# Kernel tuning notes

Measured on AMD Instinct MI355X. Metric: run time of the kernel, lower is better.

Reference implementation:

```python
import jax, jax.numpy as jnp
import numpy as np

TOKENS, IN_F, OUT_F = 8192, 4096, 4096
ZERO_POINT = 0      # input zero point (int8)
OUT_ZP = 0          # output zero point (int8)
OUT_SCALE = 0.05    # output quant scale


def setup_inputs() -> dict:
    key = jax.random.key(0)
    k1, k2, k3, k4 = jax.random.split(key, 4)
    x = jax.random.randint(k1, (TOKENS, IN_F), -128, 128, dtype=jnp.int32).astype(jnp.int8)
    # weight stored as [in_features, out_features] (module.weight.t() quantized in from_float)
    weight = jax.random.randint(k2, (IN_F, OUT_F), -127, 128, dtype=jnp.int32).astype(jnp.int8)
    bias = jax.random.randint(k3, (1, OUT_F), -1000, 1000, dtype=jnp.int32)
    gemm_scales = jax.random.uniform(k4, (1, OUT_F), minval=1e-4, maxval=2e-4, dtype=jnp.float32)
    return {"x": x, "weight": weight, "bias": bias, "gemm_scales": gemm_scales}


def reference(x, weight, bias, gemm_scales):
    # int8 -> int32 -> fp32, subtract input zero point
    a = (x.astype(jnp.int32) - ZERO_POINT).astype(jnp.float32)   # [T, IN]
    w = weight.astype(jnp.float32)                               # [IN, OUT]
    gemm_o = (a @ w + bias.astype(jnp.float32)) * gemm_scales / OUT_SCALE  # [T, OUT]
    out = jnp.clip(gemm_o + OUT_ZP, -128, 127).astype(jnp.int8)
    return out
```

## Files before the change

### kernel.cpp

```cpp
#include <hip/hip_runtime.h>
#include <stdint.h>

#define TOKENS 8192
#define IN_F   4096
#define OUT_F  4096

#define BM 256
#define BN 256
#define BK 64
#define NK (IN_F / BK)
#define THREADS 512

typedef int v4i __attribute__((ext_vector_type(4)));

#define GLOBAL_AS __attribute__((address_space(1)))
#define LDS_AS    __attribute__((address_space(3)))

__global__ __launch_bounds__(256) void pack_x_kernel(const int* __restrict__ x32,
                                                     uint8_t* __restrict__ x8) {
  int t = blockIdx.x * 256 + threadIdx.x;
  const int4 v = ((const int4*)x32)[t];
  uint32_t p = (uint32_t)(v.x & 0xFF)
             | ((uint32_t)(v.y & 0xFF) << 8)
             | ((uint32_t)(v.z & 0xFF) << 16)
             | ((uint32_t)(v.w & 0xFF) << 24);
  ((uint32_t*)x8)[t] = p;
}

__global__ __launch_bounds__(256) void packT_w_kernel(const int* __restrict__ w32,
                                                      uint8_t* __restrict__ wt8) {
  int tn = (blockIdx.x & 63) * 64;
  int tk = (blockIdx.x >> 6) * 64;
  int t = threadIdx.x;
  int n  = tn + (t >> 2);
  int k0 = tk + (t & 3) * 16;
  uint32_t words[4];
#pragma unroll
  for (int w = 0; w < 4; ++w) {
    uint32_t acc = 0;
#pragma unroll
    for (int j = 0; j < 4; ++j) {
      int val = w32[(size_t)(k0 + w * 4 + j) * OUT_F + n];
      acc |= (uint32_t)(val & 0xFF) << (8 * j);
    }
    words[w] = acc;
  }
  uint4 o = make_uint4(words[0], words[1], words[2], words[3]);
  *(uint4*)(wt8 + (size_t)n * IN_F + k0) = o;
}

__global__ __launch_bounds__(THREADS, 2) void gemm_i8_kernel(const uint8_t* __restrict__ A,
                                                             const uint8_t* __restrict__ BT,
                                                             const int* __restrict__ bias,
                                                             const float* __restrict__ scales,
                                                             int* __restrict__ out) {
  __shared__ __align__(16) uint8_t lds[4 * 32768];

  const int t    = threadIdx.x;
  const int lane = t & 63;
  const int w    = t >> 6;
  const int wr   = w >> 2;
  const int wc   = w & 3;
  const int fr   = lane & 15;
  const int fq   = lane >> 4;

  int bid = blockIdx.x;
  int swz = (bid & 7) * 64 + (bid >> 3);
  int bm = swz >> 4;
  int bn = swz & 15;

  const int lsz  = t ^ ((t >> 3) & 7);
  const int srow = lsz >> 2;
  const int scol = (lsz & 3) * 16;
  const size_t gA0 = (size_t)(bm * BM + srow) * IN_F + scol;
  const size_t gA1 = gA0 + (size_t)128 * IN_F;
  const size_t gB0 = (size_t)(bn * BN + srow) * IN_F + scol;
  const size_t gB1 = gB0 + (size_t)128 * IN_F;
  const int ldst = t * 16;

  auto stage = [&](int j) {
    uint8_t* sb = lds + (j & 3) * 32768;
    const int k0 = j * BK;
    __builtin_amdgcn_global_load_lds((const GLOBAL_AS void*)(A  + gA0 + k0),
                                     (LDS_AS void*)(sb + ldst),           16, 0, 0);
    __builtin_amdgcn_global_load_lds((const GLOBAL_AS void*)(A  + gA1 + k0),
                                     (LDS_AS void*)(sb + 8192  + ldst),   16, 0, 0);
    __builtin_amdgcn_global_load_lds((const GLOBAL_AS void*)(BT + gB0 + k0),
                                     (LDS_AS void*)(sb + 16384 + ldst),   16, 0, 0);
    __builtin_amdgcn_global_load_lds((const GLOBAL_AS void*)(BT + gB1 + k0),
                                     (LDS_AS void*)(sb + 24576 + ldst),   16, 0, 0);
  };

  int aoff[8], boff[4];
#pragma unroll
  for (int m = 0; m < 8; ++m) {
    int row = wr * 128 + m * 16 + fr;
    int half = row >> 7, rl = row & 127;
    int b = rl * 64 + fq * 16;
    b ^= ((rl >> 1) & 7) << 4;
    aoff[m] = half * 8192 + b;
  }
#pragma unroll
  for (int n = 0; n < 4; ++n) {
    int row = wc * 64 + n * 16 + fr;
    int half = row >> 7, rl = row & 127;
    int b = rl * 64 + fq * 16;
    b ^= ((rl >> 1) & 7) << 4;
    boff[n] = 16384 + half * 8192 + b;
  }

  v4i acc[8][4];
  const v4i vzero = {0, 0, 0, 0};
#pragma unroll
  for (int m = 0; m < 8; ++m)
#pragma unroll
    for (int n = 0; n < 4; ++n) acc[m][n] = vzero;

  auto compute = [&](int i) {
    const uint8_t* sb = lds + (i & 3) * 32768;
    v4i bf[4], af[4];
#pragma unroll
    for (int n = 0; n < 4; ++n) bf[n] = *(const v4i*)(sb + boff[n]);
#pragma unroll
    for (int m = 0; m < 4; ++m) af[m] = *(const v4i*)(sb + aoff[m]);
    __builtin_amdgcn_s_setprio(1);
#pragma unroll
    for (int m = 0; m < 4; ++m)
#pragma unroll
      for (int n = 0; n < 4; ++n)
        acc[m][n] = __builtin_amdgcn_mfma_i32_16x16x64_i8(af[m], bf[n], acc[m][n], 0, 0, 0);
    __builtin_amdgcn_s_setprio(0);
#pragma unroll
    for (int m = 0; m < 4; ++m) af[m] = *(const v4i*)(sb + aoff[4 + m]);
    __builtin_amdgcn_s_setprio(1);
#pragma unroll
    for (int m = 0; m < 4; ++m)
#pragma unroll
      for (int n = 0; n < 4; ++n)
        acc[4 + m][n] = __builtin_amdgcn_mfma_i32_16x16x64_i8(af[m], bf[n], acc[4 + m][n], 0, 0, 0);
    __builtin_amdgcn_s_setprio(0);
  };

  stage(0); stage(1); stage(2);

#define ITER(i, VM, DOSTAGE)                                       \
  asm volatile("s_waitcnt vmcnt(" #VM ")" ::: "memory");           \
  asm volatile("s_barrier" ::: "memory");                          \
  if (DOSTAGE) stage((i) + 3);                                     \
  __builtin_amdgcn_sched_barrier(0);                               \
  compute(i);

  for (int i = 0; i < NK - 3; ++i) {
    ITER(i, 8, true)
  }
  ITER(NK - 3, 8, false)
  ITER(NK - 2, 4, false)
  ITER(NK - 1, 0, false)
#undef ITER

#pragma unroll
  for (int n = 0; n < 4; ++n) {
    const int gn  = bn * BN + wc * 64 + n * 16 + fr;
    const int bsv = bias[gn];
    const float sc = scales[gn] * 20.0f;
#pragma unroll
    for (int m = 0; m < 8; ++m) {
      const int gm0 = bm * BM + wr * 128 + m * 16 + fq * 4;
#pragma unroll
      for (int r = 0; r < 4; ++r) {
        float g = (float)(acc[m][n][r] + bsv) * sc;
        g = fminf(fmaxf(g, -128.0f), 127.0f);
        out[(size_t)(gm0 + r) * OUT_F + gn] = (int)g;
      }
    }
  }
}

extern "C" void kernel_launch(void* const* d_in, const int* in_sizes, int n_in,
                              void* d_out, int out_size, void* d_ws, size_t ws_size,
                              hipStream_t stream) {
  const int*   x32    = (const int*)d_in[0];
  const int*   w32    = (const int*)d_in[1];
  const int*   bias   = (const int*)d_in[2];
  const float* scales = (const float*)d_in[3];
  int* out = (int*)d_out;

  uint8_t* x8  = (uint8_t*)d_ws;
  uint8_t* wt8 = (uint8_t*)d_ws + (size_t)TOKENS * IN_F;

  pack_x_kernel<<<(TOKENS * IN_F / 4) / 256, 256, 0, stream>>>(x32, x8);
  packT_w_kernel<<<(OUT_F / 64) * (IN_F / 64), 256, 0, stream>>>(w32, wt8);
  gemm_i8_kernel<<<(TOKENS / BM) * (OUT_F / BN), THREADS, 0, stream>>>(x8, wt8, bias, scales, out);
}
```

Measured before the change: 194.8 us.

## Split K-step into two barrier-separated phases interleaving A/B prefetch with MFMA

Each K iteration now runs as two phases. The A-tile prefetch is issued after the first fragment reads and the B-tile prefetch after the second, with extra workgroup barriers and lgkmcnt waits around each MFMA block. The aim is to spread global-to-LDS traffic across the compute and keep waves in lockstep, in the style of ping-pong scheduling. It adds three more barriers per iteration, which risks stalls. Because the vmcnt counts stay the same while the issue order changes, the wait thresholds still look consistent.

```diff
diff --git a/kernel.cpp b/kernel.cpp
--- a/kernel.cpp
+++ b/kernel.cpp
@@ -78,17 +78,21 @@
   const size_t gB1 = gB0 + (size_t)128 * IN_F;
   const int ldst = t * 16;
 
-  auto stage = [&](int j) {
+  auto stageA = [&](int j) {
     uint8_t* sb = lds + (j & 3) * 32768;
     const int k0 = j * BK;
-    __builtin_amdgcn_global_load_lds((const GLOBAL_AS void*)(A  + gA0 + k0),
-                                     (LDS_AS void*)(sb + ldst),           16, 0, 0);
-    __builtin_amdgcn_global_load_lds((const GLOBAL_AS void*)(A  + gA1 + k0),
-                                     (LDS_AS void*)(sb + 8192  + ldst),   16, 0, 0);
+    __builtin_amdgcn_global_load_lds((const GLOBAL_AS void*)(A + gA0 + k0),
+                                     (LDS_AS void*)(sb + ldst),          16, 0, 0);
+    __builtin_amdgcn_global_load_lds((const GLOBAL_AS void*)(A + gA1 + k0),
+                                     (LDS_AS void*)(sb + 8192 + ldst),   16, 0, 0);
+  };
+  auto stageB = [&](int j) {
+    uint8_t* sb = lds + (j & 3) * 32768;
+    const int k0 = j * BK;
     __builtin_amdgcn_global_load_lds((const GLOBAL_AS void*)(BT + gB0 + k0),
-                                     (LDS_AS void*)(sb + 16384 + ldst),   16, 0, 0);
+                                     (LDS_AS void*)(sb + 16384 + ldst),  16, 0, 0);
     __builtin_amdgcn_global_load_lds((const GLOBAL_AS void*)(BT + gB1 + k0),
-                                     (LDS_AS void*)(sb + 24576 + ldst),   16, 0, 0);
+                                     (LDS_AS void*)(sb + 24576 + ldst),  16, 0, 0);
   };
 
   int aoff[8], boff[4];
@@ -116,47 +120,50 @@
 #pragma unroll
     for (int n = 0; n < 4; ++n) acc[m][n] = vzero;
 
-  auto compute = [&](int i) {
-    const uint8_t* sb = lds + (i & 3) * 32768;
-    v4i bf[4], af[4];
-#pragma unroll
-    for (int n = 0; n < 4; ++n) bf[n] = *(const v4i*)(sb + boff[n]);
-#pragma unroll
-    for (int m = 0; m < 4; ++m) af[m] = *(const v4i*)(sb + aoff[m]);
-    __builtin_amdgcn_s_setprio(1);
-#pragma unroll
-    for (int m = 0; m < 4; ++m)
-#pragma unroll
-      for (int n = 0; n < 4; ++n)
-        acc[m][n] = __builtin_amdgcn_mfma_i32_16x16x64_i8(af[m], bf[n], acc[m][n], 0, 0, 0);
-    __builtin_amdgcn_s_setprio(0);
-#pragma unroll
-    for (int m = 0; m < 4; ++m) af[m] = *(const v4i*)(sb + aoff[4 + m]);
-    __builtin_amdgcn_s_setprio(1);
-#pragma unroll
-    for (int m = 0; m < 4; ++m)
-#pragma unroll
-      for (int n = 0; n < 4; ++n)
-        acc[4 + m][n] = __builtin_amdgcn_mfma_i32_16x16x64_i8(af[m], bf[n], acc[4 + m][n], 0, 0, 0);
-    __builtin_amdgcn_s_setprio(0);
-  };
-
-  stage(0); stage(1); stage(2);
-
-#define ITER(i, VM, DOSTAGE)                                       \
-  asm volatile("s_waitcnt vmcnt(" #VM ")" ::: "memory");           \
-  asm volatile("s_barrier" ::: "memory");                          \
-  if (DOSTAGE) stage((i) + 3);                                     \
-  __builtin_amdgcn_sched_barrier(0);                               \
-  compute(i);
+  stageA(0); stageB(0); stageA(1); stageB(1); stageA(2); stageB(2);
+
+#define SLICE(i, VM, DOSTAGE)                                                   \
+  asm volatile("s_waitcnt vmcnt(" #VM ")" ::: "memory");                        \
+  asm volatile("s_barrier" ::: "memory");                                       \
+  {                                                                             \
+    const uint8_t* sb = lds + ((i) & 3) * 32768;                                \
+    v4i bf[4], af[4], af2[4];                                                   \
+    _Pragma("unroll") for (int n = 0; n < 4; ++n)                               \
+      bf[n] = *(const v4i*)(sb + boff[n]);                                      \
+    _Pragma("unroll") for (int m = 0; m < 4; ++m)                               \
+      af[m] = *(const v4i*)(sb + aoff[m]);                                      \
+    if (DOSTAGE) stageA((i) + 3);                                               \
+    asm volatile("s_barrier" ::: "memory");                                     \
+    asm volatile("s_waitcnt lgkmcnt(0)" ::: "memory");                          \
+    __builtin_amdgcn_sched_barrier(0);                                          \
+    __builtin_amdgcn_s_setprio(1);                                              \
+    _Pragma("unroll") for (int m = 0; m < 4; ++m)                               \
+      _Pragma("unroll") for (int n = 0; n < 4; ++n)                             \
+        acc[m][n] = __builtin_amdgcn_mfma_i32_16x16x64_i8(af[m], bf[n],         \
+                                                          acc[m][n], 0, 0, 0); \
+    __builtin_amdgcn_s_setprio(0);                                              \
+    asm volatile("s_barrier" ::: "memory");                                     \
+    _Pragma("unroll") for (int m = 0; m < 4; ++m)                               \
+      af2[m] = *(const v4i*)(sb + aoff[4 + m]);                                 \
+    if (DOSTAGE) stageB((i) + 3);                                               \
+    asm volatile("s_barrier" ::: "memory");                                     \
+    asm volatile("s_waitcnt lgkmcnt(0)" ::: "memory");                          \
+    __builtin_amdgcn_sched_barrier(0);                                          \
+    __builtin_amdgcn_s_setprio(1);                                              \
+    _Pragma("unroll") for (int m = 0; m < 4; ++m)                               \
+      _Pragma("unroll") for (int n = 0; n < 4; ++n)                             \
+        acc[4 + m][n] = __builtin_amdgcn_mfma_i32_16x16x64_i8(af2[m], bf[n],    \
+                                                      acc[4 + m][n], 0, 0, 0); \
+    __builtin_amdgcn_s_setprio(0);                                              \
+  }
 
   for (int i = 0; i < NK - 3; ++i) {
-    ITER(i, 8, true)
-  }
-  ITER(NK - 3, 8, false)
-  ITER(NK - 2, 4, false)
-  ITER(NK - 1, 0, false)
-#undef ITER
+    SLICE(i, 8, true)
+  }
+  SLICE(NK - 3, 8, false)
+  SLICE(NK - 2, 4, false)
+  SLICE(NK - 1, 0, false)
+#undef SLICE
 
 #pragma unroll
   for (int n = 0; n < 4; ++n) {
```

Result: no change. 196.1 us (+0.7%).
